# Kernel tuning notes

Hardware: AMD Instinct MI355X
Metric: run time of the kernel (lower is better)

Reference implementation:

```python
import jax, jax.numpy as jnp
import numpy as np

NUM_EMBEDDINGS = 1024
EMBEDDING_DIM = 64
COMMITMENT_COST = 0.25


def setup_inputs() -> dict:
    key = jax.random.key(0)
    k1, k2 = jax.random.split(key)
    z = jax.random.normal(k1, (32, EMBEDDING_DIM, 32, 32), dtype=jnp.float32)
    # matches nn.Embedding init: uniform(-1/K, 1/K)
    codebook = jax.random.uniform(
        k2, (NUM_EMBEDDINGS, EMBEDDING_DIM), dtype=jnp.float32,
        minval=-1.0 / NUM_EMBEDDINGS, maxval=1.0 / NUM_EMBEDDINGS)
    return {"z": z, "codebook": codebook}


def reference(z, codebook):
    B, C, H, W = z.shape  # C == embedding_dim
    zp = jnp.transpose(z, (0, 2, 3, 1))          # [B,H,W,C]
    z_flat = zp.reshape(-1, C)                    # [N,C], N=B*H*W
    # squared euclidean distances to every code: [N,K]
    d = (jnp.sum(z_flat ** 2, axis=1, keepdims=True)
         + jnp.sum(codebook ** 2, axis=1)
         - 2.0 * jnp.matmul(z_flat, codebook.T))
    indices = jnp.argmin(d, axis=1)               # [N]
    z_q = codebook[indices].reshape(zp.shape)     # [B,H,W,C]
    e_latent_loss = jnp.mean((jax.lax.stop_gradient(z_q) - zp) ** 2)
    q_latent_loss = jnp.mean((z_q - jax.lax.stop_gradient(zp)) ** 2)
    loss = q_latent_loss + COMMITMENT_COST * e_latent_loss
    # straight-through estimator
    z_q_st = zp + jax.lax.stop_gradient(z_q - zp)
    z_q_out = jnp.transpose(z_q_st, (0, 3, 1, 2))  # back to NCHW
    return z_q_out, loss, indices
```

## Files before the change

kernel.cpp:

```cpp
#include <hip/hip_runtime.h>
#include <float.h>


#define DIM       64
#define N_EMB     1024
#define N_PX      32768
#define LOSS_OFF  2097152
#define IDX_OFF   2097153
#define LOSS_SCALE 5.9604644775390625e-07f

__device__ __forceinline__ float np_sumsq64_row(const float* __restrict__ row) {
    #pragma clang fp contract(off)
    float r[8];
    #pragma unroll
    for (int j = 0; j < 8; ++j) {
        float s = row[j] * row[j];
        #pragma unroll
        for (int m = 1; m < 8; ++m) {
            float p = row[j + 8 * m] * row[j + 8 * m];
            s = s + p;
        }
        r[j] = s;
    }
    return ((r[0] + r[1]) + (r[2] + r[3])) + ((r[4] + r[5]) + (r[6] + r[7]));
}

__device__ __forceinline__ float np_sumsq64_lds(const float4* ldsZ, int px) {
    #pragma clang fp contract(off)
    float4 qa = ldsZ[px];
    float4 qb = ldsZ[128 + px];
    float r0 = qa.x * qa.x, r1 = qa.y * qa.y, r2 = qa.z * qa.z, r3 = qa.w * qa.w;
    float r4 = qb.x * qb.x, r5 = qb.y * qb.y, r6 = qb.z * qb.z, r7 = qb.w * qb.w;
    #pragma unroll
    for (int m = 1; m < 8; ++m) {
        qa = ldsZ[(2 * m) * 128 + px];
        qb = ldsZ[(2 * m + 1) * 128 + px];
        float p;
        p = qa.x * qa.x; r0 = r0 + p;
        p = qa.y * qa.y; r1 = r1 + p;
        p = qa.z * qa.z; r2 = r2 + p;
        p = qa.w * qa.w; r3 = r3 + p;
        p = qb.x * qb.x; r4 = r4 + p;
        p = qb.y * qb.y; r5 = r5 + p;
        p = qb.z * qb.z; r6 = r6 + p;
        p = qb.w * qb.w; r7 = r7 + p;
    }
    return ((r0 + r1) + (r2 + r3)) + ((r4 + r5) + (r6 + r7));
}

__global__ __launch_bounds__(256, 2)
void vq_argmin(const float* __restrict__ z, const float* __restrict__ cb,
               float* __restrict__ ws_val, int* __restrict__ ws_idx,
               float* __restrict__ out) {
    __shared__ float4 ldsZ[16 * 128];
    __shared__ float4 ldsE[128 * 16];
    __shared__ float  esq[128];
    __shared__ float  cand_val[4 * 128];
    __shared__ int    cand_idx[4 * 128];

    const int tid  = threadIdx.x;
    const int lane = tid & 63;
    const int wave = __builtin_amdgcn_readfirstlane(tid >> 6);
    const int g    = blockIdx.x >> 3;
    const int s    = blockIdx.x & 7;
    const int n0   = g * 128;
    const int b    = n0 >> 10;
    const int hw0  = n0 & 1023;
    const size_t zbase = (size_t)b * 65536 + (size_t)hw0;

    {
        const int px = tid & 127;
        const int cq = tid >> 7;
        #pragma unroll
        for (int r = 0; r < 8; ++r) {
            const int c4 = cq * 8 + r;
            const float* zp = z + zbase + (size_t)(c4 * 4) * 1024 + px;
            float4 v;
            v.x = zp[0];
            v.y = zp[1024];
            v.z = zp[2048];
            v.w = zp[3072];
            ldsZ[c4 * 128 + px] = v;
        }
    }
    {
        const float4* cb4 = (const float4*)(cb + (size_t)s * 128 * DIM);
        #pragma unroll
        for (int r = 0; r < 8; ++r)
            ldsE[r * 256 + tid] = cb4[r * 256 + tid];
    }
    if (tid < 128)
        esq[tid] = np_sumsq64_row(cb + (size_t)(s * 128 + tid) * DIM);

    __syncthreads();

    const float zz0 = np_sumsq64_lds(ldsZ, lane);
    const float zz1 = np_sumsq64_lds(ldsZ, lane + 64);

    float best0 = FLT_MAX, best1 = FLT_MAX;
    int   bidx0 = 0,       bidx1 = 0;
    const int kb = s * 128 + wave * 32;
    const int lw = wave * 32;
    for (int kk = 0; kk < 32; kk += 8) {
        float d00 = 0.f, d01 = 0.f, d02 = 0.f, d03 = 0.f;
        float d04 = 0.f, d05 = 0.f, d06 = 0.f, d07 = 0.f;
        float d10 = 0.f, d11 = 0.f, d12 = 0.f, d13 = 0.f;
        float d14 = 0.f, d15 = 0.f, d16 = 0.f, d17 = 0.f;
        #pragma unroll
        for (int c4 = 0; c4 < 16; ++c4) {
            const float4 z0 = ldsZ[c4 * 128 + lane];
            const float4 z1 = ldsZ[c4 * 128 + 64 + lane];
#define VQ_CODE(J) \
            { \
                const float4 e4 = ldsE[(lw + kk + (J)) * 16 + c4];  \
                d0##J = __builtin_fmaf(e4.x, z0.x, d0##J); \
                d0##J = __builtin_fmaf(e4.y, z0.y, d0##J); \
                d0##J = __builtin_fmaf(e4.z, z0.z, d0##J); \
                d0##J = __builtin_fmaf(e4.w, z0.w, d0##J); \
                d1##J = __builtin_fmaf(e4.x, z1.x, d1##J); \
                d1##J = __builtin_fmaf(e4.y, z1.y, d1##J); \
                d1##J = __builtin_fmaf(e4.z, z1.z, d1##J); \
                d1##J = __builtin_fmaf(e4.w, z1.w, d1##J); \
            }
            VQ_CODE(0) VQ_CODE(1) VQ_CODE(2) VQ_CODE(3)
            VQ_CODE(4) VQ_CODE(5) VQ_CODE(6) VQ_CODE(7)
#undef VQ_CODE
        }
#define VQ_SCORE(J) \
        { \
            const float ee = esq[lw + kk + (J)]; \
            float sc0, sc1; \
            { \
                _Pragma("clang fp contract(off)") \
                const float p0 = zz0 + ee; \
                const float p1 = zz1 + ee; \
                sc0 = p0 - 2.0f * d0##J; \
                sc1 = p1 - 2.0f * d1##J; \
            } \
            if (sc0 < best0) { best0 = sc0; bidx0 = kb + kk + (J); } \
            if (sc1 < best1) { best1 = sc1; bidx1 = kb + kk + (J); } \
        }
        VQ_SCORE(0) VQ_SCORE(1) VQ_SCORE(2) VQ_SCORE(3)
        VQ_SCORE(4) VQ_SCORE(5) VQ_SCORE(6) VQ_SCORE(7)
#undef VQ_SCORE
    }
    cand_val[wave * 128 + lane]      = best0;
    cand_idx[wave * 128 + lane]      = bidx0;
    cand_val[wave * 128 + 64 + lane] = best1;
    cand_idx[wave * 128 + 64 + lane] = bidx1;
    __syncthreads();

    if (tid < 128) {
        float bv = cand_val[tid];
        int   bi = cand_idx[tid];
        #pragma unroll
        for (int w = 1; w < 4; ++w) {
            float v = cand_val[w * 128 + tid];
            int   i = cand_idx[w * 128 + tid];
            if (v < bv || (v == bv && i < bi)) { bv = v; bi = i; }
        }
        ws_val[s * N_PX + n0 + tid] = bv;
        ws_idx[s * N_PX + n0 + tid] = bi;
    }
    if (blockIdx.x == 0 && tid == 0) out[LOSS_OFF] = 0.f;
}

__global__ __launch_bounds__(256, 4)
void vq_out(const float* __restrict__ z, const float* __restrict__ cb,
            const float* __restrict__ ws_val, const int* __restrict__ ws_idx,
            float* __restrict__ out) {
    __shared__ int   fidx[64];
    __shared__ float lred[4];

    const int tid  = threadIdx.x;
    const int lane = tid & 63;
    const int wave = tid >> 6;
    const int n0   = blockIdx.x * 64;
    const int b    = n0 >> 10;
    const int hw0  = n0 & 1023;
    const size_t zbase = (size_t)b * 65536 + (size_t)hw0;

    if (tid < 64) {
        float bv = ws_val[n0 + tid];
        int   bi = ws_idx[n0 + tid];
        #pragma unroll
        for (int sl = 1; sl < 8; ++sl) {
            float v = ws_val[sl * N_PX + n0 + tid];
            int   i = ws_idx[sl * N_PX + n0 + tid];
            if (v < bv || (v == bv && i < bi)) { bv = v; bi = i; }
        }
        fidx[tid] = bi;
        out[IDX_OFF + n0 + tid] = (float)bi;
    }
    __syncthreads();

    const int px = tid & 63;
    const int cg = tid >> 6;
    const int mi = fidx[px];
    float lacc = 0.f;
    #pragma unroll
    for (int i = 0; i < 16; ++i) {
        const int c = cg * 16 + i;
        float q  = cb[mi * DIM + c];
        size_t go = zbase + (size_t)c * 1024 + px;
        float zv = z[go];
        float d  = q - zv;
        lacc = __builtin_fmaf(d, d, lacc);
        out[go] = q;
    }
    #pragma unroll
    for (int off = 32; off > 0; off >>= 1)
        lacc += __shfl_down(lacc, off, 64);
    if (lane == 0) lred[wave] = lacc;
    __syncthreads();
    if (tid == 0) {
        float t = (lred[0] + lred[1]) + (lred[2] + lred[3]);
        atomicAdd(&out[LOSS_OFF], t * LOSS_SCALE);
    }
}

extern "C" void kernel_launch(void* const* d_in, const int* in_sizes, int n_in,
                              void* d_out, int out_size, void* d_ws, size_t ws_size,
                              hipStream_t stream) {
    const float* z  = (const float*)d_in[0];
    const float* cb = (const float*)d_in[1];
    float* out = (float*)d_out;
    float* ws_val = (float*)d_ws;
    int*   ws_idx = (int*)((char*)d_ws + 8u * N_PX * sizeof(float));

    vq_argmin<<<2048, 256, 0, stream>>>(z, cb, ws_val, ws_idx, out);
    vq_out<<<512, 256, 0, stream>>>(z, cb, ws_val, ws_idx, out);
}
```

Measured before the change: 144.5 us.

## Enlarge argmin register tile to four pixel groups per lane with 512-thread blocks

The argmin kernel now processes 256 pixels per block with 512 threads (8 waves). Each lane accumulates dot products for 4 pixels against 8 codes per step, where before it handled 2 pixels. Each codebook float4 read from LDS is reused across twice as many pixels, which lowers LDS traffic per FMA and halves the number of blocks that reload the codebook slab. The cost is 32 accumulators per lane, which raises register pressure and may reduce occupancy, and LDS use roughly doubles for the Z tile and the candidate buffers.

```diff
diff --git a/kernel.cpp b/kernel.cpp
--- a/kernel.cpp
+++ b/kernel.cpp
@@ -9,6 +9,10 @@
 #define IDX_OFF   2097153
 #define LOSS_SCALE 5.9604644775390625e-07f
 
+#define PXT   256
+#define SLAB  128
+#define ZSTR  256
+
 __device__ __forceinline__ float np_sumsq64_row(const float* __restrict__ row) {
     #pragma clang fp contract(off)
     float r[8];
@@ -28,13 +32,13 @@
 __device__ __forceinline__ float np_sumsq64_lds(const float4* ldsZ, int px) {
     #pragma clang fp contract(off)
     float4 qa = ldsZ[px];
-    float4 qb = ldsZ[128 + px];
+    float4 qb = ldsZ[ZSTR + px];
     float r0 = qa.x * qa.x, r1 = qa.y * qa.y, r2 = qa.z * qa.z, r3 = qa.w * qa.w;
     float r4 = qb.x * qb.x, r5 = qb.y * qb.y, r6 = qb.z * qb.z, r7 = qb.w * qb.w;
     #pragma unroll
     for (int m = 1; m < 8; ++m) {
-        qa = ldsZ[(2 * m) * 128 + px];
-        qb = ldsZ[(2 * m + 1) * 128 + px];
+        qa = ldsZ[(2 * m) * ZSTR + px];
+        qb = ldsZ[(2 * m + 1) * ZSTR + px];
         float p;
         p = qa.x * qa.x; r0 = r0 + p;
         p = qa.y * qa.y; r1 = r1 + p;
@@ -48,79 +52,96 @@
     return ((r0 + r1) + (r2 + r3)) + ((r4 + r5) + (r6 + r7));
 }
 
-__global__ __launch_bounds__(256, 2)
+__global__ __launch_bounds__(512, 2)
 void vq_argmin(const float* __restrict__ z, const float* __restrict__ cb,
                float* __restrict__ ws_val, int* __restrict__ ws_idx,
                float* __restrict__ out) {
-    __shared__ float4 ldsZ[16 * 128];
-    __shared__ float4 ldsE[128 * 16];
-    __shared__ float  esq[128];
-    __shared__ float  cand_val[4 * 128];
-    __shared__ int    cand_idx[4 * 128];
+    __shared__ float4 ldsZ[16 * PXT];
+    __shared__ float4 ldsE[SLAB * 16];
+    __shared__ float  esq[SLAB];
+    __shared__ float  cand_val[8 * PXT];
+    __shared__ int    cand_idx[8 * PXT];
 
     const int tid  = threadIdx.x;
     const int lane = tid & 63;
     const int wave = __builtin_amdgcn_readfirstlane(tid >> 6);
     const int g    = blockIdx.x >> 3;
     const int s    = blockIdx.x & 7;
-    const int n0   = g * 128;
+    const int n0   = g * PXT;
     const int b    = n0 >> 10;
     const int hw0  = n0 & 1023;
     const size_t zbase = (size_t)b * 65536 + (size_t)hw0;
+    const int kb0  = s * SLAB;
 
     {
-        const int px = tid & 127;
-        const int cq = tid >> 7;
+        const int px = tid & 255;
+        const int ch = tid >> 8;
         #pragma unroll
         for (int r = 0; r < 8; ++r) {
-            const int c4 = cq * 8 + r;
+            const int c4 = ch * 8 + r;
             const float* zp = z + zbase + (size_t)(c4 * 4) * 1024 + px;
             float4 v;
             v.x = zp[0];
             v.y = zp[1024];
             v.z = zp[2048];
             v.w = zp[3072];
-            ldsZ[c4 * 128 + px] = v;
+            ldsZ[c4 * ZSTR + px] = v;
         }
     }
     {
-        const float4* cb4 = (const float4*)(cb + (size_t)s * 128 * DIM);
-        #pragma unroll
-        for (int r = 0; r < 8; ++r)
-            ldsE[r * 256 + tid] = cb4[r * 256 + tid];
-    }
-    if (tid < 128)
-        esq[tid] = np_sumsq64_row(cb + (size_t)(s * 128 + tid) * DIM);
+        const float4* cb4 = (const float4*)cb;
+        #pragma unroll
+        for (int r = 0; r < 4; ++r)
+            ldsE[r * 512 + tid] = cb4[kb0 * 16 + r * 512 + tid];
+    }
+    if (tid < SLAB)
+        esq[tid] = np_sumsq64_row(cb + (size_t)(kb0 + tid) * DIM);
 
     __syncthreads();
 
     const float zz0 = np_sumsq64_lds(ldsZ, lane);
     const float zz1 = np_sumsq64_lds(ldsZ, lane + 64);
-
-    float best0 = FLT_MAX, best1 = FLT_MAX;
-    int   bidx0 = 0,       bidx1 = 0;
-    const int kb = s * 128 + wave * 32;
-    const int lw = wave * 32;
-    for (int kk = 0; kk < 32; kk += 8) {
-        float d00 = 0.f, d01 = 0.f, d02 = 0.f, d03 = 0.f;
-        float d04 = 0.f, d05 = 0.f, d06 = 0.f, d07 = 0.f;
-        float d10 = 0.f, d11 = 0.f, d12 = 0.f, d13 = 0.f;
-        float d14 = 0.f, d15 = 0.f, d16 = 0.f, d17 = 0.f;
+    const float zz2 = np_sumsq64_lds(ldsZ, lane + 128);
+    const float zz3 = np_sumsq64_lds(ldsZ, lane + 192);
+
+    float best0 = FLT_MAX, best1 = FLT_MAX, best2 = FLT_MAX, best3 = FLT_MAX;
+    int   bidx0 = 0,       bidx1 = 0,       bidx2 = 0,       bidx3 = 0;
+    const int lw = wave * 16;
+    for (int step = 0; step < 2; ++step) {
+        const int lc = lw + step * 8;
+        float d0_0 = 0.f, d0_1 = 0.f, d0_2 = 0.f, d0_3 = 0.f;
+        float d0_4 = 0.f, d0_5 = 0.f, d0_6 = 0.f, d0_7 = 0.f;
+        float d1_0 = 0.f, d1_1 = 0.f, d1_2 = 0.f, d1_3 = 0.f;
+        float d1_4 = 0.f, d1_5 = 0.f, d1_6 = 0.f, d1_7 = 0.f;
+        float d2_0 = 0.f, d2_1 = 0.f, d2_2 = 0.f, d2_3 = 0.f;
+        float d2_4 = 0.f, d2_5 = 0.f, d2_6 = 0.f, d2_7 = 0.f;
+        float d3_0 = 0.f, d3_1 = 0.f, d3_2 = 0.f, d3_3 = 0.f;
+        float d3_4 = 0.f, d3_5 = 0.f, d3_6 = 0.f, d3_7 = 0.f;
         #pragma unroll
         for (int c4 = 0; c4 < 16; ++c4) {
-            const float4 z0 = ldsZ[c4 * 128 + lane];
-            const float4 z1 = ldsZ[c4 * 128 + 64 + lane];
+            const float4 za = ldsZ[c4 * ZSTR + lane];
+            const float4 zb = ldsZ[c4 * ZSTR + 64 + lane];
+            const float4 zc = ldsZ[c4 * ZSTR + 128 + lane];
+            const float4 zd = ldsZ[c4 * ZSTR + 192 + lane];
 #define VQ_CODE(J) \
             { \
-                const float4 e4 = ldsE[(lw + kk + (J)) * 16 + c4];  \
-                d0##J = __builtin_fmaf(e4.x, z0.x, d0##J); \
-                d0##J = __builtin_fmaf(e4.y, z0.y, d0##J); \
-                d0##J = __builtin_fmaf(e4.z, z0.z, d0##J); \
-                d0##J = __builtin_fmaf(e4.w, z0.w, d0##J); \
-                d1##J = __builtin_fmaf(e4.x, z1.x, d1##J); \
-                d1##J = __builtin_fmaf(e4.y, z1.y, d1##J); \
-                d1##J = __builtin_fmaf(e4.z, z1.z, d1##J); \
-                d1##J = __builtin_fmaf(e4.w, z1.w, d1##J); \
+                const float4 e4 = ldsE[(lc + (J)) * 16 + c4]; \
+                d0_##J = __builtin_fmaf(e4.x, za.x, d0_##J); \
+                d0_##J = __builtin_fmaf(e4.y, za.y, d0_##J); \
+                d0_##J = __builtin_fmaf(e4.z, za.z, d0_##J); \
+                d0_##J = __builtin_fmaf(e4.w, za.w, d0_##J); \
+                d1_##J = __builtin_fmaf(e4.x, zb.x, d1_##J); \
+                d1_##J = __builtin_fmaf(e4.y, zb.y, d1_##J); \
+                d1_##J = __builtin_fmaf(e4.z, zb.z, d1_##J); \
+                d1_##J = __builtin_fmaf(e4.w, zb.w, d1_##J); \
+                d2_##J = __builtin_fmaf(e4.x, zc.x, d2_##J); \
+                d2_##J = __builtin_fmaf(e4.y, zc.y, d2_##J); \
+                d2_##J = __builtin_fmaf(e4.z, zc.z, d2_##J); \
+                d2_##J = __builtin_fmaf(e4.w, zc.w, d2_##J); \
+                d3_##J = __builtin_fmaf(e4.x, zd.x, d3_##J); \
+                d3_##J = __builtin_fmaf(e4.y, zd.y, d3_##J); \
+                d3_##J = __builtin_fmaf(e4.z, zd.z, d3_##J); \
+                d3_##J = __builtin_fmaf(e4.w, zd.w, d3_##J); \
             }
             VQ_CODE(0) VQ_CODE(1) VQ_CODE(2) VQ_CODE(3)
             VQ_CODE(4) VQ_CODE(5) VQ_CODE(6) VQ_CODE(7)
@@ -128,35 +149,46 @@
         }
 #define VQ_SCORE(J) \
         { \
-            const float ee = esq[lw + kk + (J)]; \
-            float sc0, sc1; \
+            const float ee = esq[lc + (J)]; \
+            const int   ki = kb0 + lc + (J); \
+            float sc0, sc1, sc2, sc3; \
             { \
                 _Pragma("clang fp contract(off)") \
                 const float p0 = zz0 + ee; \
                 const float p1 = zz1 + ee; \
-                sc0 = p0 - 2.0f * d0##J; \
-                sc1 = p1 - 2.0f * d1##J; \
+                const float p2 = zz2 + ee; \
+                const float p3 = zz3 + ee; \
+                sc0 = p0 - 2.0f * d0_##J; \
+                sc1 = p1 - 2.0f * d1_##J; \
+                sc2 = p2 - 2.0f * d2_##J; \
+                sc3 = p3 - 2.0f * d3_##J; \
             } \
-            if (sc0 < best0) { best0 = sc0; bidx0 = kb + kk + (J); } \
-            if (sc1 < best1) { best1 = sc1; bidx1 = kb + kk + (J); } \
+            if (sc0 < best0) { best0 = sc0; bidx0 = ki; } \
+            if (sc1 < best1) { best1 = sc1; bidx1 = ki; } \
+            if (sc2 < best2) { best2 = sc2; bidx2 = ki; } \
+            if (sc3 < best3) { best3 = sc3; bidx3 = ki; } \
         }
         VQ_SCORE(0) VQ_SCORE(1) VQ_SCORE(2) VQ_SCORE(3)
         VQ_SCORE(4) VQ_SCORE(5) VQ_SCORE(6) VQ_SCORE(7)
 #undef VQ_SCORE
     }
-    cand_val[wave * 128 + lane]      = best0;
-    cand_idx[wave * 128 + lane]      = bidx0;
-    cand_val[wave * 128 + 64 + lane] = best1;
-    cand_idx[wave * 128 + 64 + lane] = bidx1;
-    __syncthreads();
-
-    if (tid < 128) {
+    cand_val[wave * PXT + lane]       = best0;
+    cand_idx[wave * PXT + lane]       = bidx0;
+    cand_val[wave * PXT + 64 + lane]  = best1;
+    cand_idx[wave * PXT + 64 + lane]  = bidx1;
+    cand_val[wave * PXT + 128 + lane] = best2;
+    cand_idx[wave * PXT + 128 + lane] = bidx2;
+    cand_val[wave * PXT + 192 + lane] = best3;
+    cand_idx[wave * PXT + 192 + lane] = bidx3;
+    __syncthreads();
+
+    if (tid < PXT) {
         float bv = cand_val[tid];
         int   bi = cand_idx[tid];
         #pragma unroll
-        for (int w = 1; w < 4; ++w) {
-            float v = cand_val[w * 128 + tid];
-            int   i = cand_idx[w * 128 + tid];
+        for (int w = 1; w < 8; ++w) {
+            float v = cand_val[w * PXT + tid];
+            int   i = cand_idx[w * PXT + tid];
             if (v < bv || (v == bv && i < bi)) { bv = v; bi = i; }
         }
         ws_val[s * N_PX + n0 + tid] = bv;
@@ -228,6 +260,6 @@
     float* ws_val = (float*)d_ws;
     int*   ws_idx = (int*)((char*)d_ws + 8u * N_PX * sizeof(float));
 
-    vq_argmin<<<2048, 256, 0, stream>>>(z, cb, ws_val, ws_idx, out);
+    vq_argmin<<<1024, 512, 0, stream>>>(z, cb, ws_val, ws_idx, out);
     vq_out<<<512, 256, 0, stream>>>(z, cb, ws_val, ws_idx, out);
 }
```

After: 257.6 us. 78.3% more time.
